# Kernel optimization log

Hardware: AMD Instinct MI355X
Metric: run time of the kernel (lower is better)

## Reference

```python
import jax, jax.numpy as jnp
import numpy as np
from jax import lax

EPS_CSA = 1e-5
EPS_BN = 1e-5


def _csa(x, w, pm_pos, ps_pos, pm_neg, ps_neg, label):
    # x: [B,C,H,W]; w: [B,K]; proto tables: [K,C]; label: [B] in {0,1}
    mean = jnp.mean(x, axis=(2, 3), keepdims=True)
    var = jnp.var(x, axis=(2, 3), ddof=1, keepdims=True)  # torch.var is unbiased
    mean = lax.stop_gradient(mean)
    var = lax.stop_gradient(var)
    x_norm = (x - mean) / jnp.sqrt(var + EPS_CSA)
    sel = (label == 0)[:, None]                       # [B,1]
    new_mean = jnp.where(sel, w @ pm_pos, w @ pm_neg)  # [B,C]
    new_std = jnp.where(sel, w @ ps_pos, w @ ps_neg)   # [B,C]
    return x_norm * new_std[:, :, None, None] + new_mean[:, :, None, None]


def _conv_bn(x, conv_w, gamma, beta):
    y = lax.conv_general_dilated(x, conv_w, (1, 1), 'SAME',
                                 dimension_numbers=('NCHW', 'OIHW', 'NCHW'))
    mu = jnp.mean(y, axis=(0, 2, 3), keepdims=True)
    var = jnp.var(y, axis=(0, 2, 3), keepdims=True)  # biased var, as BN training
    yn = (y - mu) / jnp.sqrt(var + EPS_BN)
    return yn * gamma[None, :, None, None] + beta[None, :, None, None]


def setup_inputs() -> dict:
    key = jax.random.key(0)
    ks = jax.random.split(key, 10)
    B, C, H, W, K, L = 32, 384, 32, 32, 64, 2
    conc = jnp.full((K,), 0.0156, dtype=jnp.float32)
    cw = jax.random.dirichlet(ks[5], conc, shape=(L, B)).astype(jnp.float32)
    return {
        'x': jax.random.normal(ks[0], (B, C, H, W), jnp.float32),
        'proto_mean_pos': jax.random.normal(ks[1], (L, K, C), jnp.float32),
        'proto_std_pos': jax.random.uniform(ks[2], (L, K, C), jnp.float32),
        'proto_mean_neg': jax.random.normal(ks[3], (L, K, C), jnp.float32),
        'proto_std_neg': jax.random.uniform(ks[4], (L, K, C), jnp.float32),
        'combine_weights': cw,
        'conv_w': jax.random.normal(ks[6], (C, C, 3, 3), jnp.float32) * (1.0 / np.sqrt(C * 9)),
        'bn_gamma': jnp.ones((C,), jnp.float32),
        'bn_beta': jnp.zeros((C,), jnp.float32),
        'label': jax.random.randint(ks[7], (B,), 0, 2, jnp.int32),
    }


def reference(x, proto_mean_pos, proto_std_pos, proto_mean_neg, proto_std_neg,
              combine_weights, conv_w, bn_gamma, bn_beta, label):
    fea = x
    for l in range(2):  # two CSABlocks: x + CSA(x, label)
        fea = fea + _csa(fea, combine_weights[l],
                         proto_mean_pos[l], proto_std_pos[l],
                         proto_mean_neg[l], proto_std_neg[l], label)
    out_feat = _conv_bn(fea, conv_w, bn_gamma, bn_beta)
    return out_feat
```

## Files before the change

kernel.cpp:

```cpp
#include <hip/hip_runtime.h>
#include <stdint.h>

using f32x4  = __attribute__((ext_vector_type(4))) float;
using short8 = __attribute__((ext_vector_type(8))) short;

#define DEVI static __device__ __forceinline__

DEVI unsigned short f2bf(float f) {
  unsigned u = __float_as_uint(f);
  u += 0x7FFFu + ((u >> 16) & 1u);
  return (unsigned short)(u >> 16);
}

DEVI void gld16(const void* g, void* l) {
  __builtin_amdgcn_global_load_lds(
      reinterpret_cast<const __attribute__((address_space(1))) unsigned int*>(
          reinterpret_cast<uintptr_t>(g)),
      reinterpret_cast<__attribute__((address_space(3))) unsigned int*>(
          reinterpret_cast<uintptr_t>(l)),
      16, 0, 0);
}

__global__ __launch_bounds__(256) void k_stats(const float* __restrict__ x,
                                               float* __restrict__ sums,
                                               float* __restrict__ sumsq,
                                               float* __restrict__ bn,
                                               int* __restrict__ ctr,
                                               float* __restrict__ zp) {
  const int bc = blockIdx.x;
  if (bc == 0) {
    const int t = threadIdx.x;
    for (int i = t; i < 768; i += 256) bn[i] = 0.0f;
    for (int i = t; i < 1024; i += 256) zp[i] = 0.0f;
    if (t < 4) ctr[t] = 0;
  }
  const float4 v =
      reinterpret_cast<const float4*>(x + (size_t)bc * 1024)[threadIdx.x];
  float s = v.x + v.y + v.z + v.w;
  float q = v.x * v.x + v.y * v.y + v.z * v.z + v.w * v.w;
#pragma unroll
  for (int off = 1; off < 64; off <<= 1) {
    s += __shfl_xor(s, off, 64);
    q += __shfl_xor(q, off, 64);
  }
  __shared__ float ls[4], lq[4];
  const int wv = threadIdx.x >> 6;
  if ((threadIdx.x & 63) == 0) { ls[wv] = s; lq[wv] = q; }
  __syncthreads();
  if (threadIdx.x == 0) {
    sums[bc]  = ls[0] + ls[1] + ls[2] + ls[3];
    sumsq[bc] = lq[0] + lq[1] + lq[2] + lq[3];
  }
}

__global__ __launch_bounds__(384) void k_prep(
    const float* __restrict__ w, unsigned short* __restrict__ wb2,
    const float* __restrict__ pmp, const float* __restrict__ psp,
    const float* __restrict__ pmn, const float* __restrict__ psn,
    const float* __restrict__ cw, const int* __restrict__ label,
    const float* __restrict__ sums, const float* __restrict__ sumsq,
    float* __restrict__ Ac, float* __restrict__ Bc) {
  if (blockIdx.x < 432) {
    const int g = blockIdx.x * 384 + threadIdx.x;
    const int ct = g / 41472;
    const int r1 = g - ct * 41472;
    const int step = r1 / 1152;
    const int r2 = r1 - step * 1152;
    const int slab = r2 >> 6;
    const int lane = r2 & 63;
    const int cc = step / 3, dy = step - cc * 3;
    const int r = slab * 16 + (lane >> 2);
    const int dxl = r / 96, co_l = r - dxl * 96;
    const int dd = (lane & 3) ^ ((co_l >> 1) & 3);
    const int tap = dy * 3 + dxl;
    const int co = ct * 96 + co_l;
    const int cib = cc * 32 + dd * 8;
    union { unsigned short us[8]; uint4 v4; } pk;
#pragma unroll
    for (int u = 0; u < 8; ++u)
      pk.us[u] = f2bf(w[(size_t)(co * 384 + cib + u) * 9 + tap]);
    *reinterpret_cast<uint4*>(wb2 + (size_t)g * 8) = pk.v4;
    return;
  }
  const int b = blockIdx.x - 432;
  const int c = threadIdx.x;
  __shared__ float w0[64], w1[64];
  if (threadIdx.x < 64) w0[threadIdx.x] = cw[b * 64 + threadIdx.x];
  else if (threadIdx.x < 128) w1[threadIdx.x - 64] = cw[2048 + b * 64 + (threadIdx.x - 64)];
  __syncthreads();
  const bool sel = (label[b] == 0);
  const float* m1t = (sel ? pmp : pmn);
  const float* s1t = (sel ? psp : psn);
  const float* m2t = m1t + 64 * 384;
  const float* s2t = s1t + 64 * 384;
  float m1 = 0.f, s1 = 0.f, m2 = 0.f, s2 = 0.f;
  for (int k = 0; k < 64; ++k) {
    const float a0 = w0[k], a1 = w1[k];
    m1 += a0 * m1t[k * 384 + c];
    s1 += a0 * s1t[k * 384 + c];
    m2 += a1 * m2t[k * 384 + c];
    s2 += a1 * s2t[k * 384 + c];
  }
  const int bc = b * 384 + c;
  const float sum = sums[bc], sq = sumsq[bc];
  const float mean = sum * (1.0f / 1024.0f);
  float var = (sq - sum * mean) * (1.0f / 1023.0f);
  var = fmaxf(var, 0.0f);
  const float sd1 = sqrtf(var + 1e-5f);
  const float a1c = 1.0f + s1 / sd1;
  const float b1c = m1 - mean * (s1 / sd1);
  const float mean1 = a1c * mean + b1c;
  const float var1  = a1c * a1c * var;
  const float sd2 = sqrtf(var1 + 1e-5f);
  const float t2 = 1.0f + s2 / sd2;
  Ac[bc] = a1c * t2;
  Bc[bc] = b1c * t2 + m2 - mean1 * (s2 / sd2);
}

__global__ __launch_bounds__(256) void k_fea(const float* __restrict__ x,
                                             const float* __restrict__ Ac,
                                             const float* __restrict__ Bc,
                                             unsigned short* __restrict__ fea) {
  __shared__ unsigned short tb[256][68];
  const int t = threadIdx.x;
  const int g0 = blockIdx.x << 8;
  const int b = g0 >> 10;
  const int c0 = blockIdx.y * 64;
  const float* xb = x + (((size_t)b * 384) << 10) + (g0 & 1023) + t;
  const float* Ab = Ac + b * 384 + c0;
  const float* Bb = Bc + b * 384 + c0;
#pragma unroll 1
  for (int u8 = 0; u8 < 64; u8 += 8) {
    union { unsigned short us[8]; uint4 v; } pk;
#pragma unroll
    for (int u = 0; u < 8; ++u) {
      const int c = u8 + u;
      pk.us[u] = f2bf(Ab[c] * xb[(size_t)(c0 + c) << 10] + Bb[c]);
    }
    *reinterpret_cast<uint4*>(&tb[t][u8]) = pk.v;
  }
  __syncthreads();
  const int j = t & 7;
#pragma unroll
  for (int rep = 0; rep < 8; ++rep) {
    const int p = rep * 32 + (t >> 3);
    const uint4 v = *reinterpret_cast<const uint4*>(&tb[p][j * 8]);
    *reinterpret_cast<uint4*>(fea + (size_t)(g0 + p) * 384 + c0 + j * 8) = v;
  }
}

__global__ __launch_bounds__(256, 1) void k_conv(
    const unsigned short* __restrict__ fea, const unsigned short* __restrict__ wb2,
    const unsigned short* __restrict__ zpg, float* __restrict__ out,
    float* __restrict__ bn_sum, float* __restrict__ bn_sq,
    const float* __restrict__ gamma, const float* __restrict__ beta,
    int* __restrict__ ctr) {
  __shared__ __align__(16) unsigned char lds[129024];
  const int tid = threadIdx.x;
  const int lane = tid & 63, wv = tid >> 6;
  const int pt = blockIdx.x;
  const int ct = blockIdx.y;
  const int b = pt >> 1, h0 = (pt & 1) * 16;
  const int co0 = ct * 96;
  const int wn = wv;

  const int l15 = lane & 15, d = lane >> 4;
  const int aoff = l15 * 64 + ((d ^ ((l15 >> 1) & 3)) << 4);
  int baddr[8][3];
  bool ok0[8], ok2[8];
#pragma unroll
  for (int n = 0; n < 8; ++n) {
    const int p_out = wn * 128 + n * 16 + l15;
    const int r_out = p_out >> 5, c_out = p_out & 31;
    ok0[n] = (c_out >= 1);
    ok2[n] = (c_out <= 30);
#pragma unroll
    for (int dx = 0; dx < 3; ++dx) {
      const int c = c_out + dx - 1;
      const int cs = ((unsigned)c < 32u) ? c : c_out;
      const int row = r_out * 32 + cs;
      baddr[n][dx] = row * 64 + ((d ^ ((row >> 1) & 3)) << 4);
    }
  }

  const unsigned short* wp = wb2 + (size_t)ct * 331776 + lane * 8;
#define WSTAGE(wo)                                                  \
  do {                                                              \
    gld16(wp + wv * 512,          lds + (wo) + wv * 1024);          \
    gld16(wp + wv * 512 + 2048,   lds + (wo) + wv * 1024 + 4096);   \
    gld16(wp + wv * 512 + 4096,   lds + (wo) + wv * 1024 + 8192);   \
    gld16(wp + wv * 512 + 6144,   lds + (wo) + wv * 1024 + 12288);  \
    if (wv < 2)                                                     \
      gld16(wp + wv * 512 + 8192, lds + (wo) + wv * 1024 + 16384);  \
    wp += 9216;                                                     \
  } while (0)

  const unsigned short* ip[9];
  int istep[9];
#pragma unroll
  for (int dy2 = 0; dy2 < 3; ++dy2) {
#pragma unroll
    for (int k = 0; k < 3; ++k) {
      const int j = dy2 * 3 + k;
      const int s = dy2 * 12 + wv + 4 * k;
      const int pix = s * 16 + (lane >> 2);
      const int prow = pix >> 5, pcol = pix & 31;
      const int h = h0 - 1 + prow;
      const int dd = (lane & 3) ^ ((pix >> 1) & 3);
      if (h >= 0 && h < 32) {
        ip[j] = fea + ((size_t)((b * 32 + h) * 32 + pcol) * 384 + dd * 8);
        istep[j] = 32;
      } else {
        ip[j] = zpg + lane * 8;
        istep[j] = 0;
      }
    }
  }

  f32x4 acc[6][8] = {};
  const short8 z8 = {0, 0, 0, 0, 0, 0, 0, 0};
  short8 pf_af[6], pf_bf[8];

  WSTAGE(0);
  WSTAGE(18432);
#pragma unroll
  for (int j = 0; j < 9; ++j) {
    const int dy2 = j / 3, k = j - dy2 * 3;
    const int s = dy2 * 12 + wv + 4 * k;
    gld16(ip[j], lds + 55296 + s * 1024);
    ip[j] += istep[j];
  }
  __syncthreads();
#pragma unroll
  for (int m = 0; m < 6; ++m)
    pf_af[m] = *reinterpret_cast<const short8*>(lds + m * 1024 + aoff);

  for (int cc = 0; cc < 12; ++cc) {
#pragma unroll
    for (int dy = 0; dy < 3; ++dy) {
      const int st = cc * 3 + dy;
      const unsigned char* wbase = lds + dy * 18432;
      const unsigned char* wnext = lds + ((dy + 1) % 3) * 18432;
      const unsigned char* ibase = lds + 55296 + (cc & 1) * 36864;
      if (cc < 11 || dy == 0) WSTAGE(((dy + 2) % 3) * 18432);
      if (cc < 11) {
        const int io = 55296 + ((cc + 1) & 1) * 36864;
        const int s0 = dy * 12 + wv;
#pragma unroll
        for (int k = 0; k < 3; ++k) {
          const int j = dy * 3 + k;
          gld16(ip[j], lds + io + (s0 + 4 * k) * 1024);
          ip[j] += istep[j];
        }
      }
#pragma unroll
      for (int dx = 0; dx < 3; ++dx) {
        short8 af[6], bf[8];
        if (dx == 0) {
#pragma unroll
          for (int m = 0; m < 6; ++m) af[m] = pf_af[m];
          if (dy == 0) {
#pragma unroll
            for (int n = 0; n < 8; ++n) {
              short8 v = *reinterpret_cast<const short8*>(ibase + baddr[n][0]);
              bf[n] = ok0[n] ? v : z8;
            }
          } else {
#pragma unroll
            for (int n = 0; n < 8; ++n) bf[n] = pf_bf[n];
          }
        } else {
#pragma unroll
          for (int m = 0; m < 6; ++m)
            af[m] = *reinterpret_cast<const short8*>(
                wbase + dx * 6144 + m * 1024 + aoff);
#pragma unroll
          for (int n = 0; n < 8; ++n) {
            short8 v = *reinterpret_cast<const short8*>(
                ibase + baddr[n][dx] + dy * 2048);
            if (dx == 2) v = ok2[n] ? v : z8;
            bf[n] = v;
          }
        }
#pragma unroll
        for (int m = 0; m < 6; ++m)
#pragma unroll
          for (int n = 0; n < 8; ++n)
            acc[m][n] = __builtin_amdgcn_mfma_f32_16x16x32_bf16(
                af[m], bf[n], acc[m][n], 0, 0, 0);
      }
      if (st < 35) {
#pragma unroll
        for (int m = 0; m < 6; ++m)
          pf_af[m] = *reinterpret_cast<const short8*>(wnext + m * 1024 + aoff);
        if (dy < 2) {
#pragma unroll
          for (int n = 0; n < 8; ++n) {
            short8 v = *reinterpret_cast<const short8*>(
                ibase + baddr[n][0] + (dy + 1) * 2048);
            pf_bf[n] = ok0[n] ? v : z8;
          }
        }
      }
      __syncthreads();
    }
  }
#undef WSTAGE

#pragma unroll
  for (int m = 0; m < 6; ++m) {
#pragma unroll
    for (int r = 0; r < 4; ++r) {
      const int co = m * 16 + d * 4 + r;
      float s = 0.f, q = 0.f;
#pragma unroll
      for (int n = 0; n < 8; ++n) {
        const float v = acc[m][n][r];
        s += v; q += v * v;
      }
#pragma unroll
      for (int off = 1; off < 16; off <<= 1) {
        s += __shfl_xor(s, off, 64);
        q += __shfl_xor(q, off, 64);
      }
      if (l15 == 0) {
        atomicAdd(&bn_sum[co0 + co], s);
        atomicAdd(&bn_sq[co0 + co], q);
      }
    }
  }

  float gpref = 0.f, bpref = 0.f;
  if (tid < 96) { gpref = gamma[co0 + tid]; bpref = beta[co0 + tid]; }

  __threadfence();
  __syncthreads();
  if (tid == 0) atomicAdd(&ctr[ct], 1);
  if (tid == 0) {
    while (__hip_atomic_load(&ctr[ct], __ATOMIC_ACQUIRE,
                             __HIP_MEMORY_SCOPE_AGENT) < 64)
      __builtin_amdgcn_s_sleep(2);
  }
  __syncthreads();

  float* ls_rs = reinterpret_cast<float*>(lds);
  float* ls_bb = reinterpret_cast<float*>(lds + 512);
  if (tid < 96) {
    const int co = co0 + tid;
    const float sv = __hip_atomic_load(&bn_sum[co], __ATOMIC_RELAXED,
                                       __HIP_MEMORY_SCOPE_AGENT);
    const float qv = __hip_atomic_load(&bn_sq[co], __ATOMIC_RELAXED,
                                       __HIP_MEMORY_SCOPE_AGENT);
    const float inv = 1.0f / 32768.0f;
    const float mu = sv * inv;
    const float var = fmaxf(qv * inv - mu * mu, 0.0f);
    const float rs = rsqrtf(var + 1e-5f) * gpref;
    ls_rs[tid] = rs;
    ls_bb[tid] = bpref - mu * rs;
  }
  __syncthreads();

  const size_t ob = (((size_t)b * 384 + co0) << 10) + h0 * 32;
#pragma unroll
  for (int m = 0; m < 6; ++m) {
#pragma unroll
    for (int r = 0; r < 4; ++r) {
      const int co = m * 16 + d * 4 + r;
      const float rs = ls_rs[co], bb = ls_bb[co];
#pragma unroll
      for (int n = 0; n < 8; ++n) {
        const int p = wn * 128 + n * 16 + l15;
        out[ob + ((size_t)co << 10) + p] = acc[m][n][r] * rs + bb;
      }
    }
  }
}

extern "C" void kernel_launch(void* const* d_in, const int* in_sizes, int n_in,
                              void* d_out, int out_size, void* d_ws, size_t ws_size,
                              hipStream_t stream) {
  const float* x     = (const float*)d_in[0];
  const float* pmp   = (const float*)d_in[1];
  const float* psp   = (const float*)d_in[2];
  const float* pmn   = (const float*)d_in[3];
  const float* psn   = (const float*)d_in[4];
  const float* cw    = (const float*)d_in[5];
  const float* convw = (const float*)d_in[6];
  const float* gamma = (const float*)d_in[7];
  const float* beta  = (const float*)d_in[8];
  const int*   label = (const int*)d_in[9];
  float* out = (float*)d_out;
  char* ws = (char*)d_ws;

  unsigned short* fea = (unsigned short*)(ws);
  unsigned short* wb2 = (unsigned short*)(ws + 25165824);
  float* sums  = (float*)(ws + 27820032);
  float* sumsq = (float*)(ws + 27869184);
  float* Ac    = (float*)(ws + 27918336);
  float* Bc    = (float*)(ws + 27967488);
  float* bn    = (float*)(ws + 28016640);
  float* zp    = (float*)(ws + 28019712);
  int*   ctr   = (int*)(ws + 28023808);

  k_stats<<<dim3(12288), dim3(256), 0, stream>>>(x, sums, sumsq, bn, ctr, zp);
  k_prep<<<dim3(464), dim3(384), 0, stream>>>(convw, wb2, pmp, psp, pmn, psn,
                                              cw, label, sums, sumsq, Ac, Bc);
  k_fea<<<dim3(128, 6), dim3(256), 0, stream>>>(x, Ac, Bc, fea);
  k_conv<<<dim3(64, 4), dim3(256), 0, stream>>>(fea, wb2, (const unsigned short*)zp,
                                                out, bn, bn + 384, gamma, beta, ctr);
}
```

Baseline: 154.2 us.

## Merge prep kernel into stats and fea kernels to cut a launch

The conv-weight bf16 repacking moves into the stats kernel as extra blocks. The per-(batch,channel) affine coefficient computation moves into the fea kernel, where each block computes its own 64 channels' A/B in shared memory. This removes one kernel launch and the Ac/Bc global round trip. In exchange, the prototype mixing is recomputed redundantly by the 4 spatial blocks that share each batch/channel group.

```diff
diff --git a/kernel.cpp b/kernel.cpp
--- a/kernel.cpp
+++ b/kernel.cpp
@@ -26,42 +26,12 @@
                                                float* __restrict__ sumsq,
                                                float* __restrict__ bn,
                                                int* __restrict__ ctr,
-                                               float* __restrict__ zp) {
-  const int bc = blockIdx.x;
-  if (bc == 0) {
-    const int t = threadIdx.x;
-    for (int i = t; i < 768; i += 256) bn[i] = 0.0f;
-    for (int i = t; i < 1024; i += 256) zp[i] = 0.0f;
-    if (t < 4) ctr[t] = 0;
-  }
-  const float4 v =
-      reinterpret_cast<const float4*>(x + (size_t)bc * 1024)[threadIdx.x];
-  float s = v.x + v.y + v.z + v.w;
-  float q = v.x * v.x + v.y * v.y + v.z * v.z + v.w * v.w;
-#pragma unroll
-  for (int off = 1; off < 64; off <<= 1) {
-    s += __shfl_xor(s, off, 64);
-    q += __shfl_xor(q, off, 64);
-  }
-  __shared__ float ls[4], lq[4];
-  const int wv = threadIdx.x >> 6;
-  if ((threadIdx.x & 63) == 0) { ls[wv] = s; lq[wv] = q; }
-  __syncthreads();
-  if (threadIdx.x == 0) {
-    sums[bc]  = ls[0] + ls[1] + ls[2] + ls[3];
-    sumsq[bc] = lq[0] + lq[1] + lq[2] + lq[3];
-  }
-}
-
-__global__ __launch_bounds__(384) void k_prep(
-    const float* __restrict__ w, unsigned short* __restrict__ wb2,
-    const float* __restrict__ pmp, const float* __restrict__ psp,
-    const float* __restrict__ pmn, const float* __restrict__ psn,
-    const float* __restrict__ cw, const int* __restrict__ label,
-    const float* __restrict__ sums, const float* __restrict__ sumsq,
-    float* __restrict__ Ac, float* __restrict__ Bc) {
-  if (blockIdx.x < 432) {
-    const int g = blockIdx.x * 384 + threadIdx.x;
+                                               float* __restrict__ zp,
+                                               const float* __restrict__ w,
+                                               unsigned short* __restrict__ wb2) {
+  const int bid = blockIdx.x;
+  if (bid >= 12288) {
+    const int g = (bid - 12288) * 256 + threadIdx.x;
     const int ct = g / 41472;
     const int r1 = g - ct * 41472;
     const int step = r1 / 1152;
@@ -82,60 +52,103 @@
     *reinterpret_cast<uint4*>(wb2 + (size_t)g * 8) = pk.v4;
     return;
   }
-  const int b = blockIdx.x - 432;
-  const int c = threadIdx.x;
-  __shared__ float w0[64], w1[64];
-  if (threadIdx.x < 64) w0[threadIdx.x] = cw[b * 64 + threadIdx.x];
-  else if (threadIdx.x < 128) w1[threadIdx.x - 64] = cw[2048 + b * 64 + (threadIdx.x - 64)];
-  __syncthreads();
-  const bool sel = (label[b] == 0);
-  const float* m1t = (sel ? pmp : pmn);
-  const float* s1t = (sel ? psp : psn);
-  const float* m2t = m1t + 64 * 384;
-  const float* s2t = s1t + 64 * 384;
-  float m1 = 0.f, s1 = 0.f, m2 = 0.f, s2 = 0.f;
-  for (int k = 0; k < 64; ++k) {
-    const float a0 = w0[k], a1 = w1[k];
-    m1 += a0 * m1t[k * 384 + c];
-    s1 += a0 * s1t[k * 384 + c];
-    m2 += a1 * m2t[k * 384 + c];
-    s2 += a1 * s2t[k * 384 + c];
-  }
-  const int bc = b * 384 + c;
-  const float sum = sums[bc], sq = sumsq[bc];
-  const float mean = sum * (1.0f / 1024.0f);
-  float var = (sq - sum * mean) * (1.0f / 1023.0f);
-  var = fmaxf(var, 0.0f);
-  const float sd1 = sqrtf(var + 1e-5f);
-  const float a1c = 1.0f + s1 / sd1;
-  const float b1c = m1 - mean * (s1 / sd1);
-  const float mean1 = a1c * mean + b1c;
-  const float var1  = a1c * a1c * var;
-  const float sd2 = sqrtf(var1 + 1e-5f);
-  const float t2 = 1.0f + s2 / sd2;
-  Ac[bc] = a1c * t2;
-  Bc[bc] = b1c * t2 + m2 - mean1 * (s2 / sd2);
-}
-
-__global__ __launch_bounds__(256) void k_fea(const float* __restrict__ x,
-                                             const float* __restrict__ Ac,
-                                             const float* __restrict__ Bc,
-                                             unsigned short* __restrict__ fea) {
+  const int bc = bid;
+  if (bc == 0) {
+    const int t = threadIdx.x;
+    for (int i = t; i < 768; i += 256) bn[i] = 0.0f;
+    for (int i = t; i < 1024; i += 256) zp[i] = 0.0f;
+    if (t < 4) ctr[t] = 0;
+  }
+  const float4 v =
+      reinterpret_cast<const float4*>(x + (size_t)bc * 1024)[threadIdx.x];
+  float s = v.x + v.y + v.z + v.w;
+  float q = v.x * v.x + v.y * v.y + v.z * v.z + v.w * v.w;
+#pragma unroll
+  for (int off = 1; off < 64; off <<= 1) {
+    s += __shfl_xor(s, off, 64);
+    q += __shfl_xor(q, off, 64);
+  }
+  __shared__ float ls[4], lq[4];
+  const int wv = threadIdx.x >> 6;
+  if ((threadIdx.x & 63) == 0) { ls[wv] = s; lq[wv] = q; }
+  __syncthreads();
+  if (threadIdx.x == 0) {
+    sums[bc]  = ls[0] + ls[1] + ls[2] + ls[3];
+    sumsq[bc] = lq[0] + lq[1] + lq[2] + lq[3];
+  }
+}
+
+__global__ __launch_bounds__(256) void k_fea(
+    const float* __restrict__ x, const float* __restrict__ pmp,
+    const float* __restrict__ psp, const float* __restrict__ pmn,
+    const float* __restrict__ psn, const float* __restrict__ cw,
+    const int* __restrict__ label, const float* __restrict__ sums,
+    const float* __restrict__ sumsq, unsigned short* __restrict__ fea) {
   __shared__ unsigned short tb[256][68];
+  __shared__ float w01[128];
+  __shared__ float part[4][64][4];
+  __shared__ float As[64], Bs[64];
   const int t = threadIdx.x;
   const int g0 = blockIdx.x << 8;
-  const int b = g0 >> 10;
+  const int b = blockIdx.x >> 2;
   const int c0 = blockIdx.y * 64;
+
+  if (t < 64) w01[t] = cw[b * 64 + t];
+  else if (t < 128) w01[t] = cw[2048 + b * 64 + (t - 64)];
+  __syncthreads();
+
+  {
+    const bool sel = (label[b] == 0);
+    const float* m1t = (sel ? pmp : pmn);
+    const float* s1t = (sel ? psp : psn);
+    const float* m2t = m1t + 64 * 384;
+    const float* s2t = s1t + 64 * 384;
+    const int cl = t & 63, kq = t >> 6;
+    const int c = c0 + cl;
+    float m1 = 0.f, s1 = 0.f, m2 = 0.f, s2 = 0.f;
+#pragma unroll
+    for (int i = 0; i < 16; ++i) {
+      const int k = kq * 16 + i;
+      const float a0 = w01[k], a1 = w01[64 + k];
+      m1 += a0 * m1t[k * 384 + c];
+      s1 += a0 * s1t[k * 384 + c];
+      m2 += a1 * m2t[k * 384 + c];
+      s2 += a1 * s2t[k * 384 + c];
+    }
+    part[kq][cl][0] = m1; part[kq][cl][1] = s1;
+    part[kq][cl][2] = m2; part[kq][cl][3] = s2;
+  }
+  __syncthreads();
+  if (t < 64) {
+    const float m1 = part[0][t][0] + part[1][t][0] + part[2][t][0] + part[3][t][0];
+    const float s1 = part[0][t][1] + part[1][t][1] + part[2][t][1] + part[3][t][1];
+    const float m2 = part[0][t][2] + part[1][t][2] + part[2][t][2] + part[3][t][2];
+    const float s2 = part[0][t][3] + part[1][t][3] + part[2][t][3] + part[3][t][3];
+    const int bc = b * 384 + c0 + t;
+    const float sum = sums[bc], sq = sumsq[bc];
+    const float mean = sum * (1.0f / 1024.0f);
+    float var = (sq - sum * mean) * (1.0f / 1023.0f);
+    var = fmaxf(var, 0.0f);
+    const float sd1 = sqrtf(var + 1e-5f);
+    const float a1c = 1.0f + s1 / sd1;
+    const float b1c = m1 - mean * (s1 / sd1);
+    const float mean1 = a1c * mean + b1c;
+    const float var1  = a1c * a1c * var;
+    const float sd2 = sqrtf(var1 + 1e-5f);
+    const float t2 = 1.0f + s2 / sd2;
+    As[t] = a1c * t2;
+    Bs[t] = b1c * t2 + m2 - mean1 * (s2 / sd2);
+  }
+  __syncthreads();
+
   const float* xb = x + (((size_t)b * 384) << 10) + (g0 & 1023) + t;
-  const float* Ab = Ac + b * 384 + c0;
-  const float* Bb = Bc + b * 384 + c0;
 #pragma unroll 1
   for (int u8 = 0; u8 < 64; u8 += 8) {
     union { unsigned short us[8]; uint4 v; } pk;
 #pragma unroll
     for (int u = 0; u < 8; ++u) {
       const int c = u8 + u;
-      pk.us[u] = f2bf(Ab[c] * xb[(size_t)(c0 + c) << 10] + Bb[c]);
+      pk.us[u] = f2bf(As[c] * xb[(size_t)(c0 + c) << 10] + Bs[c]);
     }
     *reinterpret_cast<uint4*>(&tb[t][u8]) = pk.v;
   }
@@ -396,16 +409,14 @@
   unsigned short* wb2 = (unsigned short*)(ws + 25165824);
   float* sums  = (float*)(ws + 27820032);
   float* sumsq = (float*)(ws + 27869184);
-  float* Ac    = (float*)(ws + 27918336);
-  float* Bc    = (float*)(ws + 27967488);
   float* bn    = (float*)(ws + 28016640);
   float* zp    = (float*)(ws + 28019712);
   int*   ctr   = (int*)(ws + 28023808);
 
-  k_stats<<<dim3(12288), dim3(256), 0, stream>>>(x, sums, sumsq, bn, ctr, zp);
-  k_prep<<<dim3(464), dim3(384), 0, stream>>>(convw, wb2, pmp, psp, pmn, psn,
-                                              cw, label, sums, sumsq, Ac, Bc);
-  k_fea<<<dim3(128, 6), dim3(256), 0, stream>>>(x, Ac, Bc, fea);
+  k_stats<<<dim3(12936), dim3(256), 0, stream>>>(x, sums, sumsq, bn, ctr, zp,
+                                                 convw, wb2);
+  k_fea<<<dim3(128, 6), dim3(256), 0, stream>>>(x, pmp, psp, pmn, psn, cw,
+                                                label, sums, sumsq, fea);
   k_conv<<<dim3(64, 4), dim3(256), 0, stream>>>(fea, wb2, (const unsigned short*)zp,
                                                 out, bn, bn + 384, gamma, beta, ctr);
 }
```

Measured after the change: 151.2 us. Within noise of the previous version (-1.9%).
